# Optimization experiments

Measured on AMD Instinct MI355X. Metric: run time of the kernel, lower is better.

Reference implementation:

```python
import jax, jax.numpy as jnp
import numpy as np

B, S, D, H = 16, 512, 512, 8
DH = D // H
EPS = 1e-5
NEG = -1.0e9


def _layernorm(v, g, b):
    mu = jnp.mean(v, axis=-1, keepdims=True)
    var = jnp.mean(jnp.square(v - mu), axis=-1, keepdims=True)
    return (v - mu) * jax.lax.rsqrt(var + EPS) * g + b


def setup_inputs() -> dict:
    key = jax.random.key(0)
    ks = jax.random.split(key, 12)
    sd = 1.0 / np.sqrt(D)
    return {
        "x": jax.random.normal(ks[0], (B, S, D), dtype=jnp.float32),
        "mask": jax.random.randint(ks[1], (B, S, S), 0, 2, dtype=jnp.int32),
        "ln_g": jnp.ones((D,), jnp.float32),
        "ln_b": jnp.zeros((D,), jnp.float32),
        "lna_g": jnp.ones((S,), jnp.float32),  # LayerNorm over attention scores (last dim = S = model_dim)
        "lna_b": jnp.zeros((S,), jnp.float32),
        "Wq": jax.random.uniform(ks[2], (D, D), jnp.float32, -sd, sd),
        "bq": jnp.zeros((D,), jnp.float32),
        "Wk": jax.random.uniform(ks[3], (D, D), jnp.float32, -sd, sd),
        "bk": jnp.zeros((D,), jnp.float32),
        "Wv": jax.random.uniform(ks[4], (D, D), jnp.float32, -sd, sd),
        "bv": jnp.zeros((D,), jnp.float32),
        "Wd": jax.random.uniform(ks[5], (D, D), jnp.float32, -sd, sd),
        "bd": jnp.zeros((D,), jnp.float32),
    }


def reference(x, mask, ln_g, ln_b, lna_g, lna_b, Wq, bq, Wk, bk, Wv, bv, Wd, bd):
    # pre-LN
    h = _layernorm(x, ln_g, ln_b)  # [B,S,D]
    # projections -> [B,H,S,DH]
    q = (h @ Wq + bq).reshape(B, S, H, DH).transpose(0, 2, 1, 3)
    k = (h @ Wk + bk).reshape(B, S, H, DH).transpose(0, 2, 1, 3)
    v = (h @ Wv + bv).reshape(B, S, H, DH).transpose(0, 2, 1, 3)
    # raw scores [B,H,S,S]
    scores = jnp.einsum("bhqd,bhkd->bhqk", q, k) / jnp.sqrt(jnp.asarray(DH, x.dtype))
    # non-standard: LayerNorm over the key axis of the score matrix
    scores = _layernorm(scores, lna_g, lna_b)
    # mask (broadcast over heads), then softmax
    scores = jnp.where(mask[:, None, :, :] == 0, jnp.asarray(NEG, x.dtype), scores)
    attn = jax.nn.softmax(scores, axis=-1)
    # dropout omitted (eval mode / deterministic reference)
    out = jnp.einsum("bhqk,bhkd->bhqd", attn, v)
    out = out.transpose(0, 2, 1, 3).reshape(B, S, D)
    out = out @ Wd + bd
    return out + x
```

## Files before the change

kernel.cpp:

```cpp
#include <hip/hip_runtime.h>
#include <hip/hip_bf16.h>
#include <stdint.h>


typedef __hip_bfloat16 bf16;
typedef __bf16 bf16x8 __attribute__((ext_vector_type(8)));
typedef float f32x4 __attribute__((ext_vector_type(4)));

#define MFMA16(a, b, c) __builtin_amdgcn_mfma_f32_16x16x32_bf16((a), (b), (c), 0, 0, 0)

static __device__ __forceinline__ bf16 f2b(float v) { return __float2bfloat16(v); }
static __device__ __forceinline__ bf16x8 ld8(const bf16* p) { return *(const bf16x8*)p; }
static __device__ __forceinline__ uint16_t f2bu(float v) {
  return __hip_bfloat16_raw(__float2bfloat16(v)).x;
}
static __device__ __forceinline__ float bu2f(uint32_t u) {
  union { uint32_t i; float f; } c;
  c.i = u << 16;
  return c.f;
}
static __device__ __forceinline__ void stage16(const bf16* g, bf16* l) {
  __builtin_amdgcn_global_load_lds(
      (const __attribute__((address_space(1))) void*)g,
      (__attribute__((address_space(3))) void*)l, 16, 0, 0);
}

__global__ __launch_bounds__(256) void prep(
    const float* __restrict__ x, const float* __restrict__ lng,
    const float* __restrict__ lnb, bf16* __restrict__ h,
    const int* __restrict__ mask, uint32_t* __restrict__ bits,
    const float* __restrict__ W0, const float* __restrict__ W1,
    const float* __restrict__ W2, const float* __restrict__ W3,
    bf16* __restrict__ T0, bf16* __restrict__ T1,
    bf16* __restrict__ T2, bf16* __restrict__ T3) {
  __shared__ float t[32][33];
  __shared__ float rs[4], rs2[4];
  const int bid = blockIdx.x;
  const int tid = threadIdx.x;

  if (bid < 8192) {
    int row = bid;
    const float* xr = x + (size_t)row * 512;
    float v0 = xr[tid], v1 = xr[tid + 256];
    float s = v0 + v1, s2 = v0 * v0 + v1 * v1;
#pragma unroll
    for (int m = 1; m < 64; m <<= 1) {
      s += __shfl_xor(s, m);
      s2 += __shfl_xor(s2, m);
    }
    int w = tid >> 6;
    if ((tid & 63) == 0) { rs[w] = s; rs2[w] = s2; }
    __syncthreads();
    s = rs[0] + rs[1] + rs[2] + rs[3];
    s2 = rs2[0] + rs2[1] + rs2[2] + rs2[3];
    float mean = s * (1.0f / 512.0f);
    float var = s2 * (1.0f / 512.0f) - mean * mean;
    float rstd = rsqrtf(var + 1e-5f);
    bf16* hr = h + (size_t)row * 512;
    hr[tid] = f2b((v0 - mean) * rstd * lng[tid] + lnb[tid]);
    hr[tid + 256] = f2b((v1 - mean) * rstd * lng[tid + 256] + lnb[tid + 256]);
  } else if (bid < 24576) {
    size_t e = (size_t)(bid - 8192) * 256 + tid;
    int mv = mask[e];
    unsigned long long bal = __ballot(mv != 0);
    if ((tid & 63) == 0) ((unsigned long long*)bits)[e >> 6] = bal;
  } else {
    int tt = bid - 24576;
    int wsel = tt >> 8, rem = tt & 255;
    int n0 = (rem & 15) * 32, k0 = (rem >> 4) * 32;
    const float* src; bf16* dst;
    switch (wsel) {
      case 0: src = W0; dst = T0; break;
      case 1: src = W1; dst = T1; break;
      case 2: src = W2; dst = T2; break;
      default: src = W3; dst = T3; break;
    }
    int tx = tid & 31, ty = tid >> 5;
#pragma unroll
    for (int i = 0; i < 4; i++) {
      int kk = ty * 4 + i;
      t[kk][tx] = src[(k0 + kk) * 512 + n0 + tx];
    }
    __syncthreads();
#pragma unroll
    for (int i = 0; i < 4; i++) {
      int nn = ty * 4 + i;
      dst[(n0 + nn) * 512 + k0 + tx] = f2b(t[tx][nn]);
    }
  }
}

__global__ __launch_bounds__(256) void gemm_qkv(
    const bf16* __restrict__ hm,
    const bf16* __restrict__ WT0, const bf16* __restrict__ WT1, const bf16* __restrict__ WT2,
    const float* __restrict__ bq, const float* __restrict__ bk, const float* __restrict__ bv,
    bf16* __restrict__ outq, bf16* __restrict__ outk, bf16* __restrict__ outvT) {
  const int sel = blockIdx.z;
  const bf16* WT = sel == 0 ? WT0 : (sel == 1 ? WT1 : WT2);
  const float* bias = sel == 0 ? bq : (sel == 1 ? bk : bv);
  __shared__ __align__(16) uint16_t SM[128 * 136];
  bf16* As = (bf16*)SM;
  bf16* Bs = (bf16*)(SM + 4096);
  int tid = threadIdx.x;
  int w = tid >> 6, lane = tid & 63, q4 = lane >> 4, l16 = lane & 15;
  int wr = w >> 1, wc = w & 1;
  int m0 = blockIdx.x * 128, n0 = blockIdx.y * 128;
  f32x4 acc[4][4];
#pragma unroll
  for (int i = 0; i < 4; i++)
#pragma unroll
    for (int j = 0; j < 4; j++) acc[i][j] = (f32x4){0.f, 0.f, 0.f, 0.f};

  for (int kc = 0; kc < 16; kc++) {
    int k0 = kc * 32;
#pragma unroll
    for (int u0 = 0; u0 < 2; u0++) {
      int e = u0 * 256 + tid;
      int row = e >> 2, c8 = (e & 3) * 8;
      stage16(&hm[(size_t)(m0 + row) * 512 + k0 + c8], &As[e * 8]);
      stage16(&WT[(size_t)(n0 + row) * 512 + k0 + c8], &Bs[e * 8]);
    }
    __syncthreads();
    bf16x8 af[4], bfr[4];
#pragma unroll
    for (int rt = 0; rt < 4; rt++)
      af[rt] = ld8(&As[(wr * 64 + rt * 16 + l16) * 32 + q4 * 8]);
#pragma unroll
    for (int nt = 0; nt < 4; nt++)
      bfr[nt] = ld8(&Bs[(wc * 64 + nt * 16 + l16) * 32 + q4 * 8]);
#pragma unroll
    for (int rt = 0; rt < 4; rt++)
#pragma unroll
      for (int nt = 0; nt < 4; nt++) acc[rt][nt] = MFMA16(af[rt], bfr[nt], acc[rt][nt]);
    __syncthreads();
  }

  if (sel != 2) {
    const float scale = sel == 0 ? 0.125f : 1.0f;
#pragma unroll
    for (int rt = 0; rt < 4; rt++)
#pragma unroll
      for (int nt = 0; nt < 4; nt++) {
        int ncol = wc * 64 + nt * 16 + l16;
        float bsv = bias[n0 + ncol];
#pragma unroll
        for (int r = 0; r < 4; r++) {
          int mrow = wr * 64 + rt * 16 + q4 * 4 + r;
          SM[mrow * 136 + ncol] = f2bu((acc[rt][nt][r] + bsv) * scale);
        }
      }
    __syncthreads();
    bf16* dst = sel == 0 ? outq : outk;
#pragma unroll
    for (int p = 0; p < 8; p++) {
      int e = p * 256 + tid;
      int row = e >> 4, c8 = (e & 15) * 8;
      bf16x8 vv = *(bf16x8*)&SM[row * 136 + c8];
      int gm = m0 + row, b_ = gm >> 9, s_ = gm & 511;
      int n = n0 + c8, hh = n >> 6, dh = n & 63;
      *(bf16x8*)(dst + ((size_t)((b_ * 8 + hh) * 512 + s_)) * 64 + dh) = vv;
    }
  } else {
#pragma unroll
    for (int rt = 0; rt < 4; rt++)
#pragma unroll
      for (int nt = 0; nt < 4; nt++) {
        int ncol = wc * 64 + nt * 16 + l16;
        float bsv = bias[n0 + ncol];
        union { uint16_t q[4]; uint2 u; } pk;
#pragma unroll
        for (int r = 0; r < 4; r++) pk.q[r] = f2bu(acc[rt][nt][r] + bsv);
        *(uint2*)&SM[ncol * 136 + wr * 64 + rt * 16 + q4 * 4] = pk.u;
      }
    __syncthreads();
#pragma unroll
    for (int p = 0; p < 8; p++) {
      int e = p * 256 + tid;
      int nn = e >> 4, s8 = (e & 15) * 8;
      bf16x8 vv = *(bf16x8*)&SM[nn * 136 + s8];
      int n = n0 + nn, hh = n >> 6, dh = n & 63;
      int gm = m0 + s8, b_ = gm >> 9, s_ = gm & 511;
      *(bf16x8*)(outvT + ((size_t)((b_ * 8 + hh) * 64 + dh)) * 512 + s_) = vv;
    }
  }
}

__global__ __launch_bounds__(256, 4) void attn_fused(
    const bf16* __restrict__ q, const bf16* __restrict__ k, const bf16* __restrict__ vT,
    const uint32_t* __restrict__ bits, const float* __restrict__ lg,
    const float* __restrict__ lb, bf16* __restrict__ ctx) {
  const int id = blockIdx.x;
  const int xcd = id & 7;
  const int j = id >> 3;
  const int mt = j & 7;
  const int bh = ((j >> 3) << 3) | xcd;
  const int m0 = mt * 64;
  const int b = bh >> 3, hh = bh & 7;
  const int tid = threadIdx.x;
  const int w = tid >> 6, lane = tid & 63, q4 = lane >> 4, l16 = lane & 15;

  __shared__ __align__(16) bf16 SBk[2][32 * 72];
  __shared__ __align__(16) bf16 SBv[2][64 * 40];
  __shared__ uint32_t GB[512];
  __shared__ uint32_t sbits[64][17];

  GB[tid] = (uint32_t)f2bu(lg[tid]) | ((uint32_t)f2bu(lb[tid]) << 16);
  GB[tid + 256] = (uint32_t)f2bu(lg[tid + 256]) | ((uint32_t)f2bu(lb[tid + 256]) << 16);
  {
    int row = tid >> 2, g = tid & 3;
    const uint32_t* src = bits + ((size_t)b * 512 + m0 + row) * 16 + g * 4;
    uint4 u = *(const uint4*)src;
    sbits[row][g * 4] = u.x; sbits[row][g * 4 + 1] = u.y;
    sbits[row][g * 4 + 2] = u.z; sbits[row][g * 4 + 3] = u.w;
  }

  const bf16* qb = q + ((size_t)bh * 512 + m0 + w * 16) * 64;
  const bf16* kb = k + (size_t)bh * 512 * 64;
  const bf16* vb = vT + (size_t)bh * 64 * 512;

  bf16x8 aq0 = ld8(qb + (size_t)l16 * 64 + q4 * 8);
  bf16x8 aq1 = ld8(qb + (size_t)l16 * 64 + 32 + q4 * 8);

  const int key0 = tid >> 3, dh8 = (tid & 7) * 8;
  const int dhv = tid >> 2, kk8 = (tid & 3) * 8;

  *(bf16x8*)&SBk[0][key0 * 72 + dh8] = ld8(kb + (size_t)key0 * 64 + dh8);
  __syncthreads();

  float s = 0.f, s2 = 0.f;
  for (int c = 0; c < 16; c++) {
    const int buf = c & 1;
    bf16x8 rk;
    if (c < 15) rk = ld8(kb + (size_t)((c + 1) * 32 + key0) * 64 + dh8);
    __builtin_amdgcn_s_setprio(1);
#pragma unroll
    for (int kg = 0; kg < 2; kg++) {
      const bf16* kp = &SBk[buf][(kg * 16 + l16) * 72];
      bf16x8 b0 = ld8(kp + q4 * 8);
      bf16x8 b1 = ld8(kp + 32 + q4 * 8);
      f32x4 acc = (f32x4){0.f, 0.f, 0.f, 0.f};
      acc = MFMA16(b0, aq0, acc);
      acc = MFMA16(b1, aq1, acc);
#pragma unroll
      for (int r = 0; r < 4; r++) {
        float v = acc[r];
        s += v;
        s2 += v * v;
      }
    }
    __builtin_amdgcn_s_setprio(0);
    if (c < 15)
      *(bf16x8*)&SBk[buf ^ 1][key0 * 72 + dh8] = rk;
    __syncthreads();
  }
  s += __shfl_xor(s, 16);  s += __shfl_xor(s, 32);
  s2 += __shfl_xor(s2, 16); s2 += __shfl_xor(s2, 32);
  const float mean = s * (1.0f / 512.0f);
  const float rstd = rsqrtf(s2 * (1.0f / 512.0f) - mean * mean + 1e-5f);

  *(bf16x8*)&SBk[0][key0 * 72 + dh8] = ld8(kb + (size_t)key0 * 64 + dh8);
  *(bf16x8*)&SBv[0][dhv * 40 + kk8] = ld8(vb + (size_t)dhv * 512 + kk8);
  __syncthreads();

  f32x4 o[4];
#pragma unroll
  for (int nt = 0; nt < 4; nt++) o[nt] = (f32x4){0.f, 0.f, 0.f, 0.f};
  float se = 0.f;
  const int src0 = ((q4 & 1) * 2) * 16 + l16;
  const int src1 = src0 + 16;
  const bool hi = (q4 >> 1) != 0;

  for (int c = 0; c < 16; c++) {
    const int buf = c & 1;
    bf16x8 rk, rv;
    if (c < 15) {
      rk = ld8(kb + (size_t)((c + 1) * 32 + key0) * 64 + dh8);
      rv = ld8(vb + (size_t)dhv * 512 + (c + 1) * 32 + kk8);
    }
    const uint32_t dw = sbits[w * 16 + l16][c];
    uint32_t Pk[2][2];
#pragma unroll
    for (int kg = 0; kg < 2; kg++) {
      const bf16* kp = &SBk[buf][(kg * 16 + l16) * 72];
      bf16x8 b0 = ld8(kp + q4 * 8);
      bf16x8 b1 = ld8(kp + 32 + q4 * 8);
      f32x4 acc = (f32x4){0.f, 0.f, 0.f, 0.f};
      __builtin_amdgcn_s_setprio(1);
      acc = MFMA16(b0, aq0, acc);
      acc = MFMA16(b1, aq1, acc);
      __builtin_amdgcn_s_setprio(0);
      uint4 gb4 = *(uint4*)&GB[c * 32 + kg * 16 + q4 * 4];
      uint16_t p[4];
#pragma unroll
      for (int r = 0; r < 4; r++) {
        uint32_t gb = r == 0 ? gb4.x : (r == 1 ? gb4.y : (r == 2 ? gb4.z : gb4.w));
        float t = (acc[r] - mean) * rstd * bu2f(gb & 0xffffu) + bu2f(gb >> 16);
        t = ((dw >> (kg * 16 + q4 * 4 + r)) & 1u) ? t : -1.0e9f;
        float pf = __expf(t);
        se += pf;
        p[r] = f2bu(pf);
      }
      Pk[kg][0] = (uint32_t)p[0] | ((uint32_t)p[1] << 16);
      Pk[kg][1] = (uint32_t)p[2] | ((uint32_t)p[3] << 16);
    }
    uint32_t t00 = __shfl(Pk[0][0], src0), t01 = __shfl(Pk[1][0], src0);
    uint32_t t10 = __shfl(Pk[0][1], src0), t11 = __shfl(Pk[1][1], src0);
    uint32_t t20 = __shfl(Pk[0][0], src1), t21 = __shfl(Pk[1][0], src1);
    uint32_t t30 = __shfl(Pk[0][1], src1), t31 = __shfl(Pk[1][1], src1);
    union { uint32_t d[4]; bf16x8 v; } af;
    af.d[0] = hi ? t01 : t00;
    af.d[1] = hi ? t11 : t10;
    af.d[2] = hi ? t21 : t20;
    af.d[3] = hi ? t31 : t30;
    __builtin_amdgcn_s_setprio(1);
#pragma unroll
    for (int nt = 0; nt < 4; nt++) {
      bf16x8 bv8 = ld8(&SBv[buf][(nt * 16 + l16) * 40 + q4 * 8]);
      o[nt] = MFMA16(af.v, bv8, o[nt]);
    }
    __builtin_amdgcn_s_setprio(0);
    if (c < 15) {
      *(bf16x8*)&SBk[buf ^ 1][key0 * 72 + dh8] = rk;
      *(bf16x8*)&SBv[buf ^ 1][dhv * 40 + kk8] = rv;
    }
    __syncthreads();
  }

  se += __shfl_xor(se, 16);
  se += __shfl_xor(se, 32);
  float invr = 1.0f / se;
  float inv[4];
#pragma unroll
  for (int r = 0; r < 4; r++) inv[r] = __shfl(invr, q4 * 4 + r);

  bf16* cb = ctx + ((size_t)b * 512 + m0 + w * 16) * 512 + hh * 64;
#pragma unroll
  for (int nt = 0; nt < 4; nt++)
#pragma unroll
    for (int r = 0; r < 4; r++)
      cb[(size_t)(q4 * 4 + r) * 512 + nt * 16 + l16] = f2b(o[nt][r] * inv[r]);
}

__global__ __launch_bounds__(256) void gemm_out(
    const bf16* __restrict__ ctx, const bf16* __restrict__ WT,
    const float* __restrict__ bd, const float* __restrict__ x, float* __restrict__ out) {
  __shared__ __align__(16) bf16 As[64 * 32];
  __shared__ __align__(16) bf16 Bs[128 * 32];
  int tid = threadIdx.x;
  int w = tid >> 6, lane = tid & 63, q4 = lane >> 4, l16 = lane & 15;
  int m0 = blockIdx.x * 64, n0 = blockIdx.y * 128;
  f32x4 acc[4][2];
#pragma unroll
  for (int i = 0; i < 4; i++)
#pragma unroll
    for (int j = 0; j < 2; j++) acc[i][j] = (f32x4){0.f, 0.f, 0.f, 0.f};

  for (int kc = 0; kc < 16; kc++) {
    int k0 = kc * 32;
    {
      int e = tid;
      int row = e >> 2, c8 = (e & 3) * 8;
      stage16(&ctx[(size_t)(m0 + row) * 512 + k0 + c8], &As[e * 8]);
    }
#pragma unroll
    for (int u0 = 0; u0 < 2; u0++) {
      int e = u0 * 256 + tid;
      int row = e >> 2, c8 = (e & 3) * 8;
      stage16(&WT[(size_t)(n0 + row) * 512 + k0 + c8], &Bs[e * 8]);
    }
    __syncthreads();
    bf16x8 af[4], bfr[2];
#pragma unroll
    for (int rt = 0; rt < 4; rt++)
      af[rt] = ld8(&As[(rt * 16 + l16) * 32 + q4 * 8]);
#pragma unroll
    for (int nt = 0; nt < 2; nt++)
      bfr[nt] = ld8(&Bs[(w * 32 + nt * 16 + l16) * 32 + q4 * 8]);
#pragma unroll
    for (int rt = 0; rt < 4; rt++)
#pragma unroll
      for (int nt = 0; nt < 2; nt++) acc[rt][nt] = MFMA16(af[rt], bfr[nt], acc[rt][nt]);
    __syncthreads();
  }
#pragma unroll
  for (int rt = 0; rt < 4; rt++) {
    int mbase = m0 + rt * 16 + q4 * 4;
#pragma unroll
    for (int nt = 0; nt < 2; nt++) {
      int n = n0 + w * 32 + nt * 16 + l16;
      float bsv = bd[n];
#pragma unroll
      for (int r = 0; r < 4; r++) {
        size_t idx = (size_t)(mbase + r) * 512 + n;
        out[idx] = acc[rt][nt][r] + bsv + x[idx];
      }
    }
  }
}

extern "C" void kernel_launch(void* const* d_in, const int* in_sizes, int n_in,
                              void* d_out, int out_size, void* d_ws, size_t ws_size,
                              hipStream_t stream) {
  const float* x = (const float*)d_in[0];
  const int* mask = (const int*)d_in[1];
  const float* ln_g = (const float*)d_in[2];
  const float* ln_b = (const float*)d_in[3];
  const float* lna_g = (const float*)d_in[4];
  const float* lna_b = (const float*)d_in[5];
  const float* Wq = (const float*)d_in[6];
  const float* bq = (const float*)d_in[7];
  const float* Wk = (const float*)d_in[8];
  const float* bk = (const float*)d_in[9];
  const float* Wv = (const float*)d_in[10];
  const float* bv = (const float*)d_in[11];
  const float* Wd = (const float*)d_in[12];
  const float* bd = (const float*)d_in[13];

  char* ws = (char*)d_ws;
  const size_t MB = 1024 * 1024;
  if (ws_size < 44 * MB) return;
  bf16* h = (bf16*)(ws);
  bf16* qd = (bf16*)(ws + 8 * MB);
  bf16* kd = (bf16*)(ws + 16 * MB);
  bf16* vTd = (bf16*)(ws + 24 * MB);
  bf16* ctx = (bf16*)(ws + 32 * MB);
  bf16* WqT = (bf16*)(ws + 40 * MB);
  bf16* WkT = (bf16*)(ws + 40 * MB + 512 * 1024);
  bf16* WvT = (bf16*)(ws + 40 * MB + 1024 * 1024);
  bf16* WdT = (bf16*)(ws + 40 * MB + 1536 * 1024);
  uint32_t* bits = (uint32_t*)(ws + 42 * MB);

  prep<<<25600, 256, 0, stream>>>(x, ln_g, ln_b, h, mask, bits,
                                  Wq, Wk, Wv, Wd, WqT, WkT, WvT, WdT);
  gemm_qkv<<<dim3(64, 4, 3), 256, 0, stream>>>(h, WqT, WkT, WvT, bq, bk, bv, qd, kd, vTd);
  attn_fused<<<1024, 256, 0, stream>>>(qd, kd, vTd, bits, lna_g, lna_b, ctx);
  gemm_out<<<dim3(128, 4), 256, 0, stream>>>(ctx, WdT, bd, x, (float*)d_out);
}
```

Before: 174.6 us.

## Compute score LayerNorm statistics algebraically from per-head K Gram matrix and key sum

Drops the first pass over all keys in the attention kernel, which computed each score row's mean and variance. Instead, the QKV GEMM builds a per-head 64x64 Gram matrix K^T K and a key-sum vector with MFMA and atomically adds them into a buffer that prep zeroes. The attention kernel then gets each row's mean as q·Kbar and its second moment as q^T M q, using a split hi/lo bf16 MFMA to keep precision. This saves one full K sweep per query tile, at the cost of extra atomics and MFMA work in the QKV GEMM. It also risks cancellation error in the E[x^2]-mean^2 variance.

```diff
diff --git a/kernel.cpp b/kernel.cpp
--- a/kernel.cpp
+++ b/kernel.cpp
@@ -32,7 +32,8 @@
     const float* __restrict__ W0, const float* __restrict__ W1,
     const float* __restrict__ W2, const float* __restrict__ W3,
     bf16* __restrict__ T0, bf16* __restrict__ T1,
-    bf16* __restrict__ T2, bf16* __restrict__ T3) {
+    bf16* __restrict__ T2, bf16* __restrict__ T3,
+    float* __restrict__ Mz) {
   __shared__ float t[32][33];
   __shared__ float rs[4], rs2[4];
   const int bid = blockIdx.x;
@@ -64,7 +65,7 @@
     int mv = mask[e];
     unsigned long long bal = __ballot(mv != 0);
     if ((tid & 63) == 0) ((unsigned long long*)bits)[e >> 6] = bal;
-  } else {
+  } else if (bid < 25600) {
     int tt = bid - 24576;
     int wsel = tt >> 8, rem = tt & 255;
     int n0 = (rem & 15) * 32, k0 = (rem >> 4) * 32;
@@ -87,6 +88,9 @@
       int nn = ty * 4 + i;
       dst[(n0 + nn) * 512 + k0 + tx] = f2b(t[tx][nn]);
     }
+  } else {
+    size_t idx = (size_t)(bid - 25600) * 256 + tid;
+    ((f32x4*)Mz)[idx] = (f32x4){0.f, 0.f, 0.f, 0.f};
   }
 }
 
@@ -94,7 +98,8 @@
     const bf16* __restrict__ hm,
     const bf16* __restrict__ WT0, const bf16* __restrict__ WT1, const bf16* __restrict__ WT2,
     const float* __restrict__ bq, const float* __restrict__ bk, const float* __restrict__ bv,
-    bf16* __restrict__ outq, bf16* __restrict__ outk, bf16* __restrict__ outvT) {
+    bf16* __restrict__ outq, bf16* __restrict__ outk, bf16* __restrict__ outvT,
+    float* __restrict__ Mbuf, float* __restrict__ Kbar) {
   const int sel = blockIdx.z;
   const bf16* WT = sel == 0 ? WT0 : (sel == 1 ? WT1 : WT2);
   const float* bias = sel == 0 ? bq : (sel == 1 ? bk : bv);
@@ -135,6 +140,65 @@
     __syncthreads();
   }
 
+  if (sel == 1) {
+#pragma unroll
+    for (int rt = 0; rt < 4; rt++)
+#pragma unroll
+      for (int nt = 0; nt < 4; nt++) {
+        int ncol = wc * 64 + nt * 16 + l16;
+        float bsv = bias[n0 + ncol];
+        union { uint16_t q[4]; uint2 u; } pk;
+#pragma unroll
+        for (int r = 0; r < 4; r++) pk.q[r] = f2bu(acc[rt][nt][r] + bsv);
+        *(uint2*)&SM[ncol * 136 + wr * 64 + rt * 16 + q4 * 4] = pk.u;
+      }
+    __syncthreads();
+    {
+      const int hloc = w & 1, itb = (w >> 1) * 2;
+      f32x4 macc[2][4], kacc[2];
+#pragma unroll
+      for (int il = 0; il < 2; il++) {
+        kacc[il] = (f32x4){0.f, 0.f, 0.f, 0.f};
+#pragma unroll
+        for (int jt = 0; jt < 4; jt++) macc[il][jt] = (f32x4){0.f, 0.f, 0.f, 0.f};
+      }
+      union { uint16_t u[8]; bf16x8 v; } ones;
+#pragma unroll
+      for (int i = 0; i < 8; i++) ones.u[i] = 0x3F80;
+#pragma unroll
+      for (int sc = 0; sc < 4; sc++) {
+        bf16x8 f[4];
+#pragma unroll
+        for (int jt = 0; jt < 4; jt++)
+          f[jt] = ld8((bf16*)&SM[(hloc * 64 + jt * 16 + l16) * 136 + sc * 32 + q4 * 8]);
+#pragma unroll
+        for (int il = 0; il < 2; il++) {
+#pragma unroll
+          for (int jt = 0; jt < 4; jt++)
+            macc[il][jt] = MFMA16(f[itb + il], f[jt], macc[il][jt]);
+          kacc[il] = MFMA16(f[itb + il], ones.v, kacc[il]);
+        }
+      }
+      const int b_ = m0 >> 9;
+      const int bhg = b_ * 8 + (n0 >> 6) + hloc;
+      float* Mp = Mbuf + (size_t)bhg * 4096;
+#pragma unroll
+      for (int il = 0; il < 2; il++) {
+        int i0 = (itb + il) * 16 + q4 * 4;
+#pragma unroll
+        for (int jt = 0; jt < 4; jt++)
+#pragma unroll
+          for (int r = 0; r < 4; r++)
+            atomicAdd(&Mp[(size_t)(i0 + r) * 64 + jt * 16 + l16], macc[il][jt][r]);
+        if (l16 == 0)
+#pragma unroll
+          for (int r = 0; r < 4; r++)
+            atomicAdd(&Kbar[(size_t)bhg * 64 + i0 + r], kacc[il][r]);
+      }
+    }
+    __syncthreads();
+  }
+
   if (sel != 2) {
     const float scale = sel == 0 ? 0.125f : 1.0f;
 #pragma unroll
@@ -187,7 +251,8 @@
 
 __global__ __launch_bounds__(256, 4) void attn_fused(
     const bf16* __restrict__ q, const bf16* __restrict__ k, const bf16* __restrict__ vT,
-    const uint32_t* __restrict__ bits, const float* __restrict__ lg,
+    const uint32_t* __restrict__ bits, const float* __restrict__ Mbuf,
+    const float* __restrict__ Kbar, const float* __restrict__ lg,
     const float* __restrict__ lb, bf16* __restrict__ ctx) {
   const int id = blockIdx.x;
   const int xcd = id & 7;
@@ -223,43 +288,69 @@
 
   const int key0 = tid >> 3, dh8 = (tid & 7) * 8;
   const int dhv = tid >> 2, kk8 = (tid & 3) * 8;
-
-  *(bf16x8*)&SBk[0][key0 * 72 + dh8] = ld8(kb + (size_t)key0 * 64 + dh8);
-  __syncthreads();
-
-  float s = 0.f, s2 = 0.f;
-  for (int c = 0; c < 16; c++) {
-    const int buf = c & 1;
-    bf16x8 rk;
-    if (c < 15) rk = ld8(kb + (size_t)((c + 1) * 32 + key0) * 64 + dh8);
-    __builtin_amdgcn_s_setprio(1);
-#pragma unroll
-    for (int kg = 0; kg < 2; kg++) {
-      const bf16* kp = &SBk[buf][(kg * 16 + l16) * 72];
-      bf16x8 b0 = ld8(kp + q4 * 8);
-      bf16x8 b1 = ld8(kp + 32 + q4 * 8);
-      f32x4 acc = (f32x4){0.f, 0.f, 0.f, 0.f};
-      acc = MFMA16(b0, aq0, acc);
-      acc = MFMA16(b1, aq1, acc);
-#pragma unroll
-      for (int r = 0; r < 4; r++) {
-        float v = acc[r];
-        s += v;
-        s2 += v * v;
-      }
-    }
-    __builtin_amdgcn_s_setprio(0);
-    if (c < 15)
-      *(bf16x8*)&SBk[buf ^ 1][key0 * 72 + dh8] = rk;
-    __syncthreads();
-  }
-  s += __shfl_xor(s, 16);  s += __shfl_xor(s, 32);
-  s2 += __shfl_xor(s2, 16); s2 += __shfl_xor(s2, 32);
-  const float mean = s * (1.0f / 512.0f);
-  const float rstd = rsqrtf(s2 * (1.0f / 512.0f) - mean * mean + 1e-5f);
-
   *(bf16x8*)&SBk[0][key0 * 72 + dh8] = ld8(kb + (size_t)key0 * 64 + dh8);
   *(bf16x8*)&SBv[0][dhv * 40 + kk8] = ld8(vb + (size_t)dhv * 512 + kk8);
+
+  float mean, rstd;
+  {
+    const float* Mb = Mbuf + (size_t)bh * 4096;
+    const float* Kb = Kbar + (size_t)bh * 64;
+    f32x4 tac[4], mn = (f32x4){0.f, 0.f, 0.f, 0.f};
+#pragma unroll
+    for (int it = 0; it < 4; it++) tac[it] = (f32x4){0.f, 0.f, 0.f, 0.f};
+#pragma unroll
+    for (int jc = 0; jc < 2; jc++) {
+      bf16x8 aq = jc ? aq1 : aq0;
+      union { uint16_t u[8]; bf16x8 v; } kh, kl;
+#pragma unroll
+      for (int e = 0; e < 8; e++) {
+        float f = Kb[jc * 32 + q4 * 8 + e];
+        kh.u[e] = f2bu(f);
+        kl.u[e] = f2bu(f - bu2f(kh.u[e]));
+      }
+      mn = MFMA16(aq, kh.v, mn);
+      mn = MFMA16(aq, kl.v, mn);
+#pragma unroll
+      for (int it = 0; it < 4; it++) {
+        const float* mp = &Mb[(size_t)(it * 16 + l16) * 64 + jc * 32 + q4 * 8];
+        union { uint16_t u[8]; bf16x8 v; } mh, ml;
+#pragma unroll
+        for (int e = 0; e < 8; e++) {
+          float f = mp[e];
+          mh.u[e] = f2bu(f);
+          ml.u[e] = f2bu(f - bu2f(mh.u[e]));
+        }
+        tac[it] = MFMA16(aq, mh.v, tac[it]);
+        tac[it] = MFMA16(aq, ml.v, tac[it]);
+      }
+    }
+    float m4[4], r4[4];
+#pragma unroll
+    for (int r = 0; r < 4; r++) {
+      float acc = 0.f;
+#pragma unroll
+      for (int it = 0; it < 4; it++) {
+        float qv = __bfloat162float(qb[(size_t)(q4 * 4 + r) * 64 + it * 16 + l16]);
+        acc += tac[it][r] * qv;
+      }
+      acc += __shfl_xor(acc, 1);
+      acc += __shfl_xor(acc, 2);
+      acc += __shfl_xor(acc, 4);
+      acc += __shfl_xor(acc, 8);
+      float me = mn[r] * (1.0f / 512.0f);
+      float va = acc * (1.0f / 512.0f) - me * me;
+      m4[r] = me;
+      r4[r] = rsqrtf(va + 1e-5f);
+    }
+    const int srcl = (l16 >> 2) << 4;
+    const int rsel = l16 & 3;
+    float t0 = __shfl(m4[0], srcl), t1 = __shfl(m4[1], srcl);
+    float t2 = __shfl(m4[2], srcl), t3 = __shfl(m4[3], srcl);
+    mean = rsel == 0 ? t0 : rsel == 1 ? t1 : rsel == 2 ? t2 : t3;
+    t0 = __shfl(r4[0], srcl); t1 = __shfl(r4[1], srcl);
+    t2 = __shfl(r4[2], srcl); t3 = __shfl(r4[3], srcl);
+    rstd = rsel == 0 ? t0 : rsel == 1 ? t1 : rsel == 2 ? t2 : t3;
+  }
   __syncthreads();
 
   f32x4 o[4];
@@ -418,7 +509,7 @@
 
   char* ws = (char*)d_ws;
   const size_t MB = 1024 * 1024;
-  if (ws_size < 44 * MB) return;
+  if (ws_size < 47 * MB) return;
   bf16* h = (bf16*)(ws);
   bf16* qd = (bf16*)(ws + 8 * MB);
   bf16* kd = (bf16*)(ws + 16 * MB);
@@ -429,10 +520,14 @@
   bf16* WvT = (bf16*)(ws + 40 * MB + 1024 * 1024);
   bf16* WdT = (bf16*)(ws + 40 * MB + 1536 * 1024);
   uint32_t* bits = (uint32_t*)(ws + 42 * MB);
-
-  prep<<<25600, 256, 0, stream>>>(x, ln_g, ln_b, h, mask, bits,
-                                  Wq, Wk, Wv, Wd, WqT, WkT, WvT, WdT);
-  gemm_qkv<<<dim3(64, 4, 3), 256, 0, stream>>>(h, WqT, WkT, WvT, bq, bk, bv, qd, kd, vTd);
-  attn_fused<<<1024, 256, 0, stream>>>(qd, kd, vTd, bits, lna_g, lna_b, ctx);
+  float* Mbuf = (float*)(ws + 44 * MB);
+  float* Kbar = (float*)(ws + 46 * MB);
+
+  prep<<<26120, 256, 0, stream>>>(x, ln_g, ln_b, h, mask, bits,
+                                  Wq, Wk, Wv, Wd, WqT, WkT, WvT, WdT, Mbuf);
+  gemm_qkv<<<dim3(64, 4, 3), 256, 0, stream>>>(h, WqT, WkT, WvT, bq, bk, bv,
+                                               qd, kd, vTd, Mbuf, Kbar);
+  attn_fused<<<1024, 256, 0, stream>>>(qd, kd, vTd, bits, Mbuf, Kbar,
+                                       lna_g, lna_b, ctx);
   gemm_out<<<dim3(128, 4), 256, 0, stream>>>(ctx, WdT, bd, x, (float*)d_out);
 }
```

New measurement: 212.6 us. 1.22x slower.

## Load K and V fragments directly from global memory, dropping LDS double-buffering

Applied to the files above, without the earlier changes.

Removes the shared-memory double-buffered staging of K and V tiles and the per-iteration block barriers. Each wave now reads its MFMA operands straight from global memory (relying on L1/L2 caching) and adds unroll pragmas to expose more loads in flight. This cuts LDS traffic, LDS footprint and synchronisation. The cost is that the four waves each fetch the same K/V data redundantly and global latency is no longer hidden by explicit prefetch.

```diff
diff --git a/kernel.cpp b/kernel.cpp
--- a/kernel.cpp
+++ b/kernel.cpp
@@ -199,8 +199,6 @@
   const int tid = threadIdx.x;
   const int w = tid >> 6, lane = tid & 63, q4 = lane >> 4, l16 = lane & 15;
 
-  __shared__ __align__(16) bf16 SBk[2][32 * 72];
-  __shared__ __align__(16) bf16 SBv[2][64 * 40];
   __shared__ uint32_t GB[512];
   __shared__ uint32_t sbits[64][17];
 
@@ -221,26 +219,21 @@
   bf16x8 aq0 = ld8(qb + (size_t)l16 * 64 + q4 * 8);
   bf16x8 aq1 = ld8(qb + (size_t)l16 * 64 + 32 + q4 * 8);
 
-  const int key0 = tid >> 3, dh8 = (tid & 7) * 8;
-  const int dhv = tid >> 2, kk8 = (tid & 3) * 8;
-
-  *(bf16x8*)&SBk[0][key0 * 72 + dh8] = ld8(kb + (size_t)key0 * 64 + dh8);
   __syncthreads();
 
   float s = 0.f, s2 = 0.f;
+#pragma unroll 4
   for (int c = 0; c < 16; c++) {
-    const int buf = c & 1;
-    bf16x8 rk;
-    if (c < 15) rk = ld8(kb + (size_t)((c + 1) * 32 + key0) * 64 + dh8);
-    __builtin_amdgcn_s_setprio(1);
 #pragma unroll
     for (int kg = 0; kg < 2; kg++) {
-      const bf16* kp = &SBk[buf][(kg * 16 + l16) * 72];
+      const bf16* kp = kb + (size_t)(c * 32 + kg * 16 + l16) * 64;
       bf16x8 b0 = ld8(kp + q4 * 8);
       bf16x8 b1 = ld8(kp + 32 + q4 * 8);
       f32x4 acc = (f32x4){0.f, 0.f, 0.f, 0.f};
+      __builtin_amdgcn_s_setprio(1);
       acc = MFMA16(b0, aq0, acc);
       acc = MFMA16(b1, aq1, acc);
+      __builtin_amdgcn_s_setprio(0);
 #pragma unroll
       for (int r = 0; r < 4; r++) {
         float v = acc[r];
@@ -248,19 +241,11 @@
         s2 += v * v;
       }
     }
-    __builtin_amdgcn_s_setprio(0);
-    if (c < 15)
-      *(bf16x8*)&SBk[buf ^ 1][key0 * 72 + dh8] = rk;
-    __syncthreads();
   }
   s += __shfl_xor(s, 16);  s += __shfl_xor(s, 32);
   s2 += __shfl_xor(s2, 16); s2 += __shfl_xor(s2, 32);
   const float mean = s * (1.0f / 512.0f);
   const float rstd = rsqrtf(s2 * (1.0f / 512.0f) - mean * mean + 1e-5f);
-
-  *(bf16x8*)&SBk[0][key0 * 72 + dh8] = ld8(kb + (size_t)key0 * 64 + dh8);
-  *(bf16x8*)&SBv[0][dhv * 40 + kk8] = ld8(vb + (size_t)dhv * 512 + kk8);
-  __syncthreads();
 
   f32x4 o[4];
 #pragma unroll
@@ -270,18 +255,13 @@
   const int src1 = src0 + 16;
   const bool hi = (q4 >> 1) != 0;
 
+#pragma unroll 2
   for (int c = 0; c < 16; c++) {
-    const int buf = c & 1;
-    bf16x8 rk, rv;
-    if (c < 15) {
-      rk = ld8(kb + (size_t)((c + 1) * 32 + key0) * 64 + dh8);
-      rv = ld8(vb + (size_t)dhv * 512 + (c + 1) * 32 + kk8);
-    }
     const uint32_t dw = sbits[w * 16 + l16][c];
     uint32_t Pk[2][2];
 #pragma unroll
     for (int kg = 0; kg < 2; kg++) {
-      const bf16* kp = &SBk[buf][(kg * 16 + l16) * 72];
+      const bf16* kp = kb + (size_t)(c * 32 + kg * 16 + l16) * 64;
       bf16x8 b0 = ld8(kp + q4 * 8);
       bf16x8 b1 = ld8(kp + 32 + q4 * 8);
       f32x4 acc = (f32x4){0.f, 0.f, 0.f, 0.f};
@@ -315,15 +295,10 @@
     __builtin_amdgcn_s_setprio(1);
 #pragma unroll
     for (int nt = 0; nt < 4; nt++) {
-      bf16x8 bv8 = ld8(&SBv[buf][(nt * 16 + l16) * 40 + q4 * 8]);
+      bf16x8 bv8 = ld8(vb + (size_t)(nt * 16 + l16) * 512 + c * 32 + q4 * 8);
       o[nt] = MFMA16(af.v, bv8, o[nt]);
     }
     __builtin_amdgcn_s_setprio(0);
-    if (c < 15) {
-      *(bf16x8*)&SBk[buf ^ 1][key0 * 72 + dh8] = rk;
-      *(bf16x8*)&SBv[buf ^ 1][dhv * 40 + kk8] = rv;
-    }
-    __syncthreads();
   }
 
   se += __shfl_xor(se, 16);
```

Measured after the change: 232.3 us. 1.33x slower.
